# Kernel optimization log

Hardware: AMD Instinct MI355X
Metric: run time of the kernel (lower is better)

Reference implementation:

```python
import jax, jax.numpy as jnp
import numpy as np

B, S = 2, 1024
V, D, H, L, F, M = 50257, 768, 12, 6, 3072, 1024
DK = D // H
EPS = 1e-5


def _layer_norm(x, g, b):
    mu = jnp.mean(x, axis=-1, keepdims=True)
    var = jnp.mean(jnp.square(x - mu), axis=-1, keepdims=True)
    return (x - mu) * jax.lax.rsqrt(var + EPS) * g + b


def setup_inputs() -> dict:
    key = jax.random.key(0)
    ks = jax.random.split(key, 20)
    std = 0.02
    inp = {
        'input_ids': jax.random.randint(ks[0], (B, S), 0, V),
        'tok_emb': jax.random.normal(ks[1], (V, D), jnp.float32) * std,
        'pos_emb': jax.random.normal(ks[2], (M, D), jnp.float32) * std,
        # per-layer stacked params; linear weights stored as [in, out] (y = x @ W)
        'wq': jax.random.normal(ks[3], (L, D, D), jnp.float32) * std,
        'wk': jax.random.normal(ks[4], (L, D, D), jnp.float32) * std,
        'wv': jax.random.normal(ks[5], (L, D, D), jnp.float32) * std,
        'wo': jax.random.normal(ks[6], (L, D, D), jnp.float32) * std,
        'bo': jnp.zeros((L, D), jnp.float32),
        'fc_w': jax.random.normal(ks[7], (L, D, F), jnp.float32) * std,
        'fc_b': jnp.zeros((L, F), jnp.float32),
        'proj_w': jax.random.normal(ks[8], (L, F, D), jnp.float32) * std,
        'proj_b': jnp.zeros((L, D), jnp.float32),
        'ln1_g': jnp.ones((L, D), jnp.float32),
        'ln1_b': jnp.zeros((L, D), jnp.float32),
        'ln2_g': jnp.ones((L, D), jnp.float32),
        'ln2_b': jnp.zeros((L, D), jnp.float32),
        'lnf_g': jnp.ones((D,), jnp.float32),
        'lnf_b': jnp.zeros((D,), jnp.float32),
        'out_w': jax.random.normal(ks[9], (D, V), jnp.float32) * std,
    }
    return inp


def reference(input_ids, tok_emb, pos_emb, wq, wk, wv, wo, bo, fc_w, fc_b,
              proj_w, proj_b, ln1_g, ln1_b, ln2_g, ln2_b, lnf_g, lnf_b, out_w):
    b, s = input_ids.shape
    x = tok_emb[input_ids] + pos_emb[jnp.arange(s)][None, :, :]  # [B,S,D]
    causal = jnp.tril(jnp.ones((s, s), bool))  # [S,S]
    scale = 1.0 / np.sqrt(DK)
    for l in range(L):
        xn = _layer_norm(x, ln1_g[l], ln1_b[l])
        q = (xn @ wq[l]).reshape(b, s, H, DK).transpose(0, 2, 1, 3)
        k = (xn @ wk[l]).reshape(b, s, H, DK).transpose(0, 2, 1, 3)
        v = (xn @ wv[l]).reshape(b, s, H, DK).transpose(0, 2, 1, 3)
        scores = jnp.einsum('bhqd,bhkd->bhqk', q, k) * scale
        scores = jnp.where(causal[None, None], scores, -1e9)
        attn = jax.nn.softmax(scores, axis=-1)
        ctx = jnp.einsum('bhqk,bhkd->bhqd', attn, v)
        ctx = ctx.transpose(0, 2, 1, 3).reshape(b, s, D)
        x = x + ctx @ wo[l] + bo[l]
        xn = _layer_norm(x, ln2_g[l], ln2_b[l])
        h = jax.nn.gelu(xn @ fc_w[l] + fc_b[l], approximate=False)
        x = x + h @ proj_w[l] + proj_b[l]
    x = _layer_norm(x, lnf_g, lnf_b)
    logits = x @ out_w  # [B,S,V]
    return logits
```

## Files before the change

kernel.cpp:

```cpp
#include <hip/hip_runtime.h>
#include <hip/hip_bf16.h>
#include <math.h>

#define BB 2
#define SS 1024
#define DD 768
#define HH 12
#define LL 6
#define FF 3072
#define VV 50257
#define DKK 64
#define NROWS (BB * SS)
#define QKVN (3 * DD)
#define QBLK 64
#define KVBLK 64

#define OFF_QKV 0
#define OFF_WO  1769472
#define OFF_FC  2359296
#define OFF_PROJ 4718592
#define PL      7077888

typedef __attribute__((ext_vector_type(8))) short short8v;
typedef __attribute__((ext_vector_type(4))) float f32x4;
typedef __attribute__((ext_vector_type(4))) int int4v;

__device__ __forceinline__ float gelu_f(float x) {
    return 0.5f * x * (1.0f + erff(x * 0.70710678118654752440f));
}

__global__ __launch_bounds__(256) void embed_kernel(
    const int* __restrict__ ids, const float* __restrict__ tok,
    const float* __restrict__ pos, float* __restrict__ x) {
    int row = blockIdx.x;
    int s = row & (SS - 1);
    int id = ids[row];
    const float* t = tok + (size_t)id * DD;
    const float* p = pos + (size_t)s * DD;
    float* xr = x + (size_t)row * DD;
    for (int i = threadIdx.x; i < DD; i += 256)
        xr[i] = t[i] + p[i];
}

__global__ __launch_bounds__(256) void ln_kernel(
    const float* __restrict__ x, const float* __restrict__ g,
    const float* __restrict__ b, float* __restrict__ out) {
    int row = blockIdx.x;
    int tid = threadIdx.x;
    const float* xr = x + (size_t)row * DD;
    float v0 = xr[tid], v1 = xr[tid + 256], v2 = xr[tid + 512];
    __shared__ float red[256];
    red[tid] = v0 + v1 + v2;
    __syncthreads();
    for (int s2 = 128; s2 > 0; s2 >>= 1) {
        if (tid < s2) red[tid] += red[tid + s2];
        __syncthreads();
    }
    float mu = red[0] * (1.0f / DD);
    __syncthreads();
    float d0 = v0 - mu, d1 = v1 - mu, d2 = v2 - mu;
    red[tid] = d0 * d0 + d1 * d1 + d2 * d2;
    __syncthreads();
    for (int s2 = 128; s2 > 0; s2 >>= 1) {
        if (tid < s2) red[tid] += red[tid + s2];
        __syncthreads();
    }
    float r = rsqrtf(red[0] * (1.0f / DD) + 1e-5f);
    float* o = out + (size_t)row * DD;
    o[tid]       = d0 * r * g[tid]       + b[tid];
    o[tid + 256] = d1 * r * g[tid + 256] + b[tid + 256];
    o[tid + 512] = d2 * r * g[tid + 512] + b[tid + 512];
}

__global__ __launch_bounds__(256) void ln_bf16_kernel(
    const float* __restrict__ x, const float* __restrict__ g,
    const float* __restrict__ b, __hip_bfloat16* __restrict__ out) {
    int row = blockIdx.x;
    int tid = threadIdx.x;
    const float* xr = x + (size_t)row * DD;
    float v0 = xr[tid], v1 = xr[tid + 256], v2 = xr[tid + 512];
    __shared__ float red[256];
    red[tid] = v0 + v1 + v2;
    __syncthreads();
    for (int s2 = 128; s2 > 0; s2 >>= 1) {
        if (tid < s2) red[tid] += red[tid + s2];
        __syncthreads();
    }
    float mu = red[0] * (1.0f / DD);
    __syncthreads();
    float d0 = v0 - mu, d1 = v1 - mu, d2 = v2 - mu;
    red[tid] = d0 * d0 + d1 * d1 + d2 * d2;
    __syncthreads();
    for (int s2 = 128; s2 > 0; s2 >>= 1) {
        if (tid < s2) red[tid] += red[tid + s2];
        __syncthreads();
    }
    float r = rsqrtf(red[0] * (1.0f / DD) + 1e-5f);
    __hip_bfloat16* o = out + (size_t)row * DD;
    o[tid]       = __float2bfloat16(d0 * r * g[tid]       + b[tid]);
    o[tid + 256] = __float2bfloat16(d1 * r * g[tid + 256] + b[tid + 256]);
    o[tid + 512] = __float2bfloat16(d2 * r * g[tid + 512] + b[tid + 512]);
}

__global__ __launch_bounds__(256) void transpose_cvt_kernel(
    const float* __restrict__ W, __hip_bfloat16* __restrict__ Wt, int K, int N) {
    __shared__ float t[32][33];
    int bn = blockIdx.x * 32, bk = blockIdx.y * 32;
    int tx = threadIdx.x & 31, ty = threadIdx.x >> 5;
    for (int r = ty; r < 32; r += 8)
        t[r][tx] = (bn + tx < N) ? W[(size_t)(bk + r) * N + bn + tx] : 0.0f;
    __syncthreads();
    for (int r = ty; r < 32; r += 8) {
        int n = bn + r;
        if (n < N) Wt[(size_t)n * K + bk + tx] = __float2bfloat16(t[tx][r]);
    }
}

__global__ __launch_bounds__(256) void transpose_all_kernel(
    const float* __restrict__ wq, const float* __restrict__ wk,
    const float* __restrict__ wv, const float* __restrict__ wo,
    const float* __restrict__ fc_w, const float* __restrict__ proj_w,
    const float* __restrict__ out_w, __hip_bfloat16* __restrict__ Wt_all) {
    int bid = blockIdx.x;
    const float* W;
    __hip_bfloat16* Wt;
    int K, N, tn, tk;
    if (bid < 6 * 6912) {
        int l = bid / 6912, r = bid % 6912;
        __hip_bfloat16* base = Wt_all + (size_t)l * PL;
        if (r < 1728) {
            int which = r / 576, idx = r % 576;
            W = (which == 0 ? wq : (which == 1 ? wk : wv)) + (size_t)l * DD * DD;
            Wt = base + (size_t)which * DD * DD;
            K = DD; N = DD; tn = idx % 24; tk = idx / 24;
        } else if (r < 2304) {
            int idx = r - 1728;
            W = wo + (size_t)l * DD * DD;
            Wt = base + OFF_WO;
            K = DD; N = DD; tn = idx % 24; tk = idx / 24;
        } else if (r < 4608) {
            int idx = r - 2304;
            W = fc_w + (size_t)l * DD * FF;
            Wt = base + OFF_FC;
            K = DD; N = FF; tn = idx % 96; tk = idx / 96;
        } else {
            int idx = r - 4608;
            W = proj_w + (size_t)l * FF * DD;
            Wt = base + OFF_PROJ;
            K = FF; N = DD; tn = idx % 24; tk = idx / 24;
        }
    } else {
        int idx = bid - 6 * 6912;
        W = out_w;
        Wt = Wt_all + (size_t)6 * PL;
        K = DD; N = VV; tn = idx % 1571; tk = idx / 1571;
    }
    __shared__ float t[32][33];
    int bn = tn * 32, bk = tk * 32;
    int tx = threadIdx.x & 31, ty = threadIdx.x >> 5;
    for (int r = ty; r < 32; r += 8)
        t[r][tx] = (bn + tx < N) ? W[(size_t)(bk + r) * N + bn + tx] : 0.0f;
    __syncthreads();
    for (int r = ty; r < 32; r += 8) {
        int n = bn + r;
        if (n < N) Wt[(size_t)n * K + bk + tx] = __float2bfloat16(t[tx][r]);
    }
}

#define LDSOFF(row, ks) (((row) * 64) + ((((ks) ^ (((row) >> 1) & 3))) << 4))
#define SWZ128(row, byteoff) \
    ((row) * 128 + (((((byteoff) >> 4) ^ ((row) & 7)) & 7) << 4) + ((byteoff) & 15))

__device__ __forceinline__ void tile_remap(int mtiles, int BM, int BN, int& bm, int& bn) {
    const int nblk = gridDim.x;
    int hw = blockIdx.x, j = hw;
    if ((nblk & 7) == 0) j = (hw & 7) * (nblk >> 3) + (hw >> 3);
    bm = (j % mtiles) * BM;
    bn = (j / mtiles) * BN;
}

template<int BM, int BN>
__global__ __launch_bounds__(256) void gemm_mfma_kernel(
    const __hip_bfloat16* __restrict__ A, const __hip_bfloat16* __restrict__ Wt,
    const float* __restrict__ bias, const float* __restrict__ residual,
    float* __restrict__ Cf, __hip_bfloat16* __restrict__ Cb,
    int M, int N, int K, int do_gelu, int mtiles) {
    constexpr int BK = 32;
    constexpr int UA = (BM * 4) / 256;
    constexpr int UB = (BN * 4) / 256;
    constexpr int FM = BM / 32;
    constexpr int FN = BN / 32;
    __shared__ __align__(16) char As[BM * 64];
    __shared__ __align__(16) char Bs[BN * 64];

    const int tid = threadIdx.x;
    const int lane = tid & 63;
    const int wid = tid >> 6;
    int bm, bn;
    tile_remap(mtiles, BM, BN, bm, bn);
    const int r16 = lane & 15;
    const int kg = lane >> 4;
    const int wm = (wid >> 1) * (FM * 16);
    const int wn = (wid & 1) * (FN * 16);

    f32x4 acc[FM][FN];
    const f32x4 zf = {0.0f, 0.0f, 0.0f, 0.0f};
#pragma unroll
    for (int i = 0; i < FM; ++i)
#pragma unroll
        for (int j = 0; j < FN; ++j) acc[i][j] = zf;

    int4v areg[UA], breg[UB];
    const int4v zi = {0, 0, 0, 0};

#pragma unroll
    for (int u = 0; u < UA; ++u) {
        int c = tid + u * 256, row = c >> 2, sl = c & 3;
        areg[u] = *(const int4v*)(A + (size_t)(bm + row) * K + sl * 8);
    }
#pragma unroll
    for (int u = 0; u < UB; ++u) {
        int c = tid + u * 256, row = c >> 2, sl = c & 3;
        int4v bv = zi;
        if (bn + row < N) bv = *(const int4v*)(Wt + (size_t)(bn + row) * K + sl * 8);
        breg[u] = bv;
    }

    for (int k0 = 0; k0 < K; k0 += BK) {
        __syncthreads();
#pragma unroll
        for (int u = 0; u < UA; ++u) {
            int c = tid + u * 256, row = c >> 2, sl = c & 3;
            *(int4v*)(As + LDSOFF(row, sl)) = areg[u];
        }
#pragma unroll
        for (int u = 0; u < UB; ++u) {
            int c = tid + u * 256, row = c >> 2, sl = c & 3;
            *(int4v*)(Bs + LDSOFF(row, sl)) = breg[u];
        }
        __syncthreads();
        int kn = k0 + BK;
        if (kn < K) {
#pragma unroll
            for (int u = 0; u < UA; ++u) {
                int c = tid + u * 256, row = c >> 2, sl = c & 3;
                areg[u] = *(const int4v*)(A + (size_t)(bm + row) * K + kn + sl * 8);
            }
#pragma unroll
            for (int u = 0; u < UB; ++u) {
                int c = tid + u * 256, row = c >> 2, sl = c & 3;
                int4v bv = zi;
                if (bn + row < N) bv = *(const int4v*)(Wt + (size_t)(bn + row) * K + kn + sl * 8);
                breg[u] = bv;
            }
        }
        short8v af[FM], bfr[FN];
#pragma unroll
        for (int i = 0; i < FM; ++i) {
            int row = wm + i * 16 + r16;
            af[i] = *(const short8v*)(As + LDSOFF(row, kg));
        }
#pragma unroll
        for (int j = 0; j < FN; ++j) {
            int row = wn + j * 16 + r16;
            bfr[j] = *(const short8v*)(Bs + LDSOFF(row, kg));
        }
#pragma unroll
        for (int i = 0; i < FM; ++i)
#pragma unroll
            for (int j = 0; j < FN; ++j)
                acc[i][j] = __builtin_amdgcn_mfma_f32_16x16x32_bf16(
                    af[i], bfr[j], acc[i][j], 0, 0, 0);
    }

    const int rg = lane >> 4;
#pragma unroll
    for (int i = 0; i < FM; ++i) {
#pragma unroll
        for (int j = 0; j < FN; ++j) {
            int col = bn + wn + j * 16 + r16;
            if (col < N) {
#pragma unroll
                for (int r = 0; r < 4; ++r) {
                    int row = bm + wm + i * 16 + rg * 4 + r;
                    float v = acc[i][j][r];
                    if (bias) v += bias[col];
                    if (do_gelu) v = gelu_f(v);
                    size_t o = (size_t)row * N + col;
                    if (residual) v += residual[o];
                    if (Cf) Cf[o] = v;
                    else Cb[o] = __float2bfloat16(v);
                }
            }
        }
    }
}

__global__ __launch_bounds__(256) void qkv_gemm_kernel(
    const __hip_bfloat16* __restrict__ A, const __hip_bfloat16* __restrict__ Wt,
    __hip_bfloat16* __restrict__ qh, __hip_bfloat16* __restrict__ kh,
    __hip_bfloat16* __restrict__ vt) {
    constexpr int BM = 128, BN = 128, BK = 32;
    constexpr int K = DD;
    constexpr int UA = 2, UB = 2, FM = 4, FN = 4;
    __shared__ __align__(16) char As[BM * 64];
    __shared__ __align__(16) char Bs[BN * 64];

    const int tid = threadIdx.x;
    const int lane = tid & 63;
    const int wid = tid >> 6;
    int bm, bn;
    tile_remap(16, BM, BN, bm, bn);
    const int r16 = lane & 15;
    const int kg = lane >> 4;
    const int wm = (wid >> 1) * 64;
    const int wn = (wid & 1) * 64;

    f32x4 acc[FM][FN];
    const f32x4 zf = {0.0f, 0.0f, 0.0f, 0.0f};
#pragma unroll
    for (int i = 0; i < FM; ++i)
#pragma unroll
        for (int j = 0; j < FN; ++j) acc[i][j] = zf;

    int4v areg[UA], breg[UB];
#pragma unroll
    for (int u = 0; u < UA; ++u) {
        int c = tid + u * 256, row = c >> 2, sl = c & 3;
        areg[u] = *(const int4v*)(A + (size_t)(bm + row) * K + sl * 8);
    }
#pragma unroll
    for (int u = 0; u < UB; ++u) {
        int c = tid + u * 256, row = c >> 2, sl = c & 3;
        breg[u] = *(const int4v*)(Wt + (size_t)(bn + row) * K + sl * 8);
    }

    for (int k0 = 0; k0 < K; k0 += BK) {
        __syncthreads();
#pragma unroll
        for (int u = 0; u < UA; ++u) {
            int c = tid + u * 256, row = c >> 2, sl = c & 3;
            *(int4v*)(As + LDSOFF(row, sl)) = areg[u];
        }
#pragma unroll
        for (int u = 0; u < UB; ++u) {
            int c = tid + u * 256, row = c >> 2, sl = c & 3;
            *(int4v*)(Bs + LDSOFF(row, sl)) = breg[u];
        }
        __syncthreads();
        int kn = k0 + BK;
        if (kn < K) {
#pragma unroll
            for (int u = 0; u < UA; ++u) {
                int c = tid + u * 256, row = c >> 2, sl = c & 3;
                areg[u] = *(const int4v*)(A + (size_t)(bm + row) * K + kn + sl * 8);
            }
#pragma unroll
            for (int u = 0; u < UB; ++u) {
                int c = tid + u * 256, row = c >> 2, sl = c & 3;
                breg[u] = *(const int4v*)(Wt + (size_t)(bn + row) * K + kn + sl * 8);
            }
        }
        short8v af[FM], bfr[FN];
#pragma unroll
        for (int i = 0; i < FM; ++i)
            af[i] = *(const short8v*)(As + LDSOFF(wm + i * 16 + r16, kg));
#pragma unroll
        for (int j = 0; j < FN; ++j)
            bfr[j] = *(const short8v*)(Bs + LDSOFF(wn + j * 16 + r16, kg));
#pragma unroll
        for (int i = 0; i < FM; ++i)
#pragma unroll
            for (int j = 0; j < FN; ++j)
                acc[i][j] = __builtin_amdgcn_mfma_f32_16x16x32_bf16(
                    af[i], bfr[j], acc[i][j], 0, 0, 0);
    }

#pragma unroll
    for (int i = 0; i < FM; ++i) {
#pragma unroll
        for (int j = 0; j < FN; ++j) {
            int col = bn + wn + j * 16 + r16;
#pragma unroll
            for (int r = 0; r < 4; ++r) {
                int row = bm + wm + i * 16 + kg * 4 + r;
                int b = row >> 10, s = row & (SS - 1);
                float v = acc[i][j][r];
                if (col < DD) {
                    int h = col >> 6, d = col & 63;
                    qh[((size_t)(b * HH + h) * SS + s) * DKK + d] =
                        __float2bfloat16(v * 0.125f);
                } else if (col < 2 * DD) {
                    int c = col - DD, h = c >> 6, d = c & 63;
                    kh[((size_t)(b * HH + h) * SS + s) * DKK + d] = __float2bfloat16(v);
                } else {
                    int c = col - 2 * DD, h = c >> 6, d = c & 63;
                    vt[((size_t)(b * HH + h) * DKK + d) * SS + s] = __float2bfloat16(v);
                }
            }
        }
    }
}

__global__ __launch_bounds__(256) void flash_attn_kernel(
    const __hip_bfloat16* __restrict__ qh, const __hip_bfloat16* __restrict__ kh,
    const __hip_bfloat16* __restrict__ vt, __hip_bfloat16* __restrict__ ctx) {
    __shared__ __align__(16) char Ks[KVBLK * 128];
    __shared__ __align__(16) char Vs[DKK * 128];
    __shared__ __align__(16) char Ps[4][16 * 128];

    const int bh = blockIdx.x;
    const int qt = (gridDim.y - 1) - blockIdx.y;
    const int q0 = qt * QBLK;
    const int b = bh / HH;
    const int h = bh - b * HH;
    const int tid = threadIdx.x;
    const int lane = tid & 63;
    const int w = tid >> 6;
    const int r16 = lane & 15;
    const int kg = lane >> 4;
    char* Pw = Ps[w];

    const size_t qbase = ((size_t)bh * SS + q0 + w * 16 + r16) * DKK;
    short8v qf0 = *(const short8v*)(qh + qbase + kg * 8);
    short8v qf1 = *(const short8v*)(qh + qbase + 32 + kg * 8);

    f32x4 acc_o[4];
    const f32x4 zf = {0.0f, 0.0f, 0.0f, 0.0f};
    float m[4], l[4];
#pragma unroll
    for (int j = 0; j < 4; ++j) acc_o[j] = zf;
#pragma unroll
    for (int r = 0; r < 4; ++r) { m[r] = -1e30f; l[r] = 0.0f; }

    const int nt = qt + 1;
    for (int t = 0; t < nt; ++t) {
        __syncthreads();
        {
            const __hip_bfloat16* kp = kh + ((size_t)bh * SS + t * KVBLK) * DKK;
            const __hip_bfloat16* vp = vt + (size_t)bh * DKK * SS + t * KVBLK;
#pragma unroll
            for (int u = 0; u < 2; ++u) {
                int c = tid + u * 256;
                int row = c >> 3, slot = c & 7;
                *(int4v*)(Ks + SWZ128(row, slot * 16)) =
                    *(const int4v*)(kp + (size_t)row * DKK + slot * 8);
                *(int4v*)(Vs + SWZ128(row, slot * 16)) =
                    *(const int4v*)(vp + (size_t)row * SS + slot * 8);
            }
        }
        __syncthreads();

        f32x4 s[4];
#pragma unroll
        for (int j = 0; j < 4; ++j) s[j] = zf;
#pragma unroll
        for (int j = 0; j < 4; ++j) {
            short8v k0f = *(const short8v*)(Ks + SWZ128(j * 16 + r16, kg * 16));
            short8v k1f = *(const short8v*)(Ks + SWZ128(j * 16 + r16, 64 + kg * 16));
            s[j] = __builtin_amdgcn_mfma_f32_16x16x32_bf16(qf0, k0f, s[j], 0, 0, 0);
            s[j] = __builtin_amdgcn_mfma_f32_16x16x32_bf16(qf1, k1f, s[j], 0, 0, 0);
        }

        if (t == qt) {
#pragma unroll
            for (int j = 0; j < 4; ++j)
#pragma unroll
                for (int r = 0; r < 4; ++r)
                    if (j * 16 + r16 > w * 16 + kg * 4 + r) s[j][r] = -1e30f;
        }

        float alpha[4], rsum[4];
#pragma unroll
        for (int r = 0; r < 4; ++r) {
            float v = fmaxf(fmaxf(s[0][r], s[1][r]), fmaxf(s[2][r], s[3][r]));
#pragma unroll
            for (int d2 = 1; d2 < 16; d2 <<= 1)
                v = fmaxf(v, __shfl_xor(v, d2));
            float mnew = fmaxf(m[r], v);
            alpha[r] = __expf(m[r] - mnew);
            m[r] = mnew;
            rsum[r] = 0.0f;
        }
#pragma unroll
        for (int j = 0; j < 4; ++j)
#pragma unroll
            for (int r = 0; r < 4; ++r) {
                float p = __expf(s[j][r] - m[r]);
                rsum[r] += p;
                *(__hip_bfloat16*)(Pw + SWZ128(kg * 4 + r, (j * 16 + r16) * 2)) =
                    __float2bfloat16(p);
            }
#pragma unroll
        for (int r = 0; r < 4; ++r) {
#pragma unroll
            for (int d2 = 1; d2 < 16; d2 <<= 1)
                rsum[r] += __shfl_xor(rsum[r], d2);
            l[r] = l[r] * alpha[r] + rsum[r];
        }
#pragma unroll
        for (int j = 0; j < 4; ++j)
#pragma unroll
            for (int r = 0; r < 4; ++r) acc_o[j][r] *= alpha[r];

        short8v pa0 = *(const short8v*)(Pw + SWZ128(r16, kg * 16));
        short8v pa1 = *(const short8v*)(Pw + SWZ128(r16, 64 + kg * 16));
#pragma unroll
        for (int j = 0; j < 4; ++j) {
            short8v v0f = *(const short8v*)(Vs + SWZ128(j * 16 + r16, kg * 16));
            short8v v1f = *(const short8v*)(Vs + SWZ128(j * 16 + r16, 64 + kg * 16));
            acc_o[j] = __builtin_amdgcn_mfma_f32_16x16x32_bf16(pa0, v0f, acc_o[j], 0, 0, 0);
            acc_o[j] = __builtin_amdgcn_mfma_f32_16x16x32_bf16(pa1, v1f, acc_o[j], 0, 0, 0);
        }
    }

#pragma unroll
    for (int r = 0; r < 4; ++r) {
        float inv = 1.0f / l[r];
        int row = q0 + w * 16 + kg * 4 + r;
        __hip_bfloat16* cp = ctx + ((size_t)(b * SS) + row) * DD + h * DKK;
#pragma unroll
        for (int j = 0; j < 4; ++j)
            cp[j * 16 + r16] = __float2bfloat16(acc_o[j][r] * inv);
    }
}

__global__ __launch_bounds__(256) void gemm_kernel(
    const float* __restrict__ A, const float* __restrict__ W,
    const float* __restrict__ bias, const float* __restrict__ residual,
    float* __restrict__ C, int M, int N, int K, int do_gelu) {
    __shared__ float As[16][64];
    __shared__ float Ws[16][68];
    int tid = threadIdx.x;
    int bn = blockIdx.x * 64, bm = blockIdx.y * 64;
    int tx = tid & 15, ty = tid >> 4;
    int ar = tid >> 2, ak = (tid & 3) << 2;
    int wr = tid >> 4, wc = (tid & 15) << 2;
    bool n_vec = ((N & 3) == 0);
    float acc[4][4] = {};
    for (int k0 = 0; k0 < K; k0 += 16) {
        float4 av = *(const float4*)&A[(size_t)(bm + ar) * K + (k0 + ak)];
        As[ak + 0][ar] = av.x; As[ak + 1][ar] = av.y;
        As[ak + 2][ar] = av.z; As[ak + 3][ar] = av.w;
        int gn = bn + wc;
        const float* wp = &W[(size_t)(k0 + wr) * N + gn];
        float w0, w1, w2, w3;
        if (n_vec && gn + 3 < N) {
            float4 wv4 = *(const float4*)wp;
            w0 = wv4.x; w1 = wv4.y; w2 = wv4.z; w3 = wv4.w;
        } else {
            w0 = (gn + 0 < N) ? wp[0] : 0.0f;
            w1 = (gn + 1 < N) ? wp[1] : 0.0f;
            w2 = (gn + 2 < N) ? wp[2] : 0.0f;
            w3 = (gn + 3 < N) ? wp[3] : 0.0f;
        }
        Ws[wr][wc + 0] = w0; Ws[wr][wc + 1] = w1;
        Ws[wr][wc + 2] = w2; Ws[wr][wc + 3] = w3;
        __syncthreads();
#pragma unroll
        for (int kk = 0; kk < 16; ++kk) {
            float a[4], w[4];
#pragma unroll
            for (int i = 0; i < 4; ++i) a[i] = As[kk][ty * 4 + i];
#pragma unroll
            for (int j = 0; j < 4; ++j) w[j] = Ws[kk][tx * 4 + j];
#pragma unroll
            for (int i = 0; i < 4; ++i)
#pragma unroll
                for (int j = 0; j < 4; ++j)
                    acc[i][j] = fmaf(a[i], w[j], acc[i][j]);
        }
        __syncthreads();
    }
#pragma unroll
    for (int i = 0; i < 4; ++i) {
        int row = bm + ty * 4 + i;
#pragma unroll
        for (int j = 0; j < 4; ++j) {
            int col = bn + tx * 4 + j;
            if (col < N) {
                float val = acc[i][j];
                if (bias) val += bias[col];
                if (do_gelu) val = gelu_f(val);
                if (residual) val += residual[(size_t)row * N + col];
                C[(size_t)row * N + col] = val;
            }
        }
    }
}

__global__ __launch_bounds__(256) void attn_kernel(
    const float* __restrict__ q, const float* __restrict__ k,
    const float* __restrict__ v, float* __restrict__ ctx) {
    int bid = blockIdx.x;
    int qi = bid & (SS - 1);
    int bh = bid >> 10;
    int h = bh % HH;
    int b = bh / HH;
    int tid = threadIdx.x;
    __shared__ float qs[DKK];
    __shared__ float p[SS];
    __shared__ float red[256];
    __shared__ float ctx_red[4][DKK];
    const float* qrow = q + ((size_t)(b * SS + qi)) * DD + h * DKK;
    if (tid < DKK) qs[tid] = qrow[tid];
    __syncthreads();
    int nk = qi + 1;
    const float scale = 0.125f;
    for (int ki = tid; ki < nk; ki += 256) {
        const float* krow = k + ((size_t)(b * SS + ki)) * DD + h * DKK;
        float dot = 0.0f;
#pragma unroll
        for (int d = 0; d < DKK; d += 4) {
            float4 kv = *(const float4*)&krow[d];
            dot += qs[d] * kv.x + qs[d + 1] * kv.y + qs[d + 2] * kv.z + qs[d + 3] * kv.w;
        }
        p[ki] = dot * scale;
    }
    __syncthreads();
    float lmax = -1e30f;
    for (int ki = tid; ki < nk; ki += 256) lmax = fmaxf(lmax, p[ki]);
    red[tid] = lmax;
    __syncthreads();
    for (int s2 = 128; s2 > 0; s2 >>= 1) {
        if (tid < s2) red[tid] = fmaxf(red[tid], red[tid + s2]);
        __syncthreads();
    }
    float mm = red[0];
    __syncthreads();
    float lsum = 0.0f;
    for (int ki = tid; ki < nk; ki += 256) {
        float e = __expf(p[ki] - mm);
        p[ki] = e;
        lsum += e;
    }
    red[tid] = lsum;
    __syncthreads();
    for (int s2 = 128; s2 > 0; s2 >>= 1) {
        if (tid < s2) red[tid] += red[tid + s2];
        __syncthreads();
    }
    float inv = 1.0f / red[0];
    int d = tid & 63;
    int chunk = tid >> 6;
    float accd = 0.0f;
    for (int ki = chunk; ki < nk; ki += 4)
        accd += p[ki] * v[((size_t)(b * SS + ki)) * DD + h * DKK + d];
    ctx_red[chunk][d] = accd;
    __syncthreads();
    if (tid < DKK) {
        float sum = (ctx_red[0][tid] + ctx_red[1][tid]) + (ctx_red[2][tid] + ctx_red[3][tid]);
        ctx[((size_t)(b * SS + qi)) * DD + h * DKK + tid] = sum * inv;
    }
}

extern "C" void kernel_launch(void* const* d_in, const int* in_sizes, int n_in,
                              void* d_out, int out_size, void* d_ws, size_t ws_size,
                              hipStream_t stream) {
    const int*   ids    = (const int*)  d_in[0];
    const float* tok    = (const float*)d_in[1];
    const float* pos    = (const float*)d_in[2];
    const float* wq     = (const float*)d_in[3];
    const float* wk     = (const float*)d_in[4];
    const float* wv     = (const float*)d_in[5];
    const float* wo     = (const float*)d_in[6];
    const float* bo     = (const float*)d_in[7];
    const float* fc_w   = (const float*)d_in[8];
    const float* fc_b   = (const float*)d_in[9];
    const float* proj_w = (const float*)d_in[10];
    const float* proj_b = (const float*)d_in[11];
    const float* ln1_g  = (const float*)d_in[12];
    const float* ln1_b  = (const float*)d_in[13];
    const float* ln2_g  = (const float*)d_in[14];
    const float* ln2_b  = (const float*)d_in[15];
    const float* lnf_g  = (const float*)d_in[16];
    const float* lnf_b  = (const float*)d_in[17];
    const float* out_w  = (const float*)d_in[18];
    float* out = (float*)d_out;

    dim3 blk(256);

    const size_t SZ_X    = (size_t)NROWS * DD * 4;
    const size_t SZ_XN   = (size_t)NROWS * DD * 2;
    const size_t SZ_HD   = (size_t)BB * HH * SS * DKK * 2;
    const size_t SZ_CTX  = (size_t)NROWS * DD * 2;
    const size_t SZ_H    = (size_t)NROWS * FF * 2;
    const size_t SZ_WT1  = (size_t)50304 * DD * 2;
    const size_t SZ_WTA  = ((size_t)6 * PL + (size_t)50304 * DD) * 2;
    const size_t ACT     = SZ_X + SZ_XN + 3 * SZ_HD + SZ_CTX + SZ_H;
    const size_t NEED_MID = ACT + SZ_WT1;
    const size_t NEED_BIG = ACT + SZ_WTA;

    if (ws_size >= NEED_MID) {
        const bool big = (ws_size >= NEED_BIG);
        char* p = (char*)d_ws;
        float*          x    = (float*)p;          p += SZ_X;
        __hip_bfloat16* xn   = (__hip_bfloat16*)p; p += SZ_XN;
        __hip_bfloat16* qhb  = (__hip_bfloat16*)p; p += SZ_HD;
        __hip_bfloat16* khb  = (__hip_bfloat16*)p; p += SZ_HD;
        __hip_bfloat16* vtb  = (__hip_bfloat16*)p; p += SZ_HD;
        __hip_bfloat16* ctx  = (__hip_bfloat16*)p; p += SZ_CTX;
        __hip_bfloat16* hbuf = (__hip_bfloat16*)p; p += SZ_H;
        __hip_bfloat16* Wt   = (__hip_bfloat16*)p;

        dim3 tD(DD / 32, DD / 32);
        dim3 tF(FF / 32, DD / 32);
        dim3 tP(DD / 32, FF / 32);
        dim3 tV((VV + 31) / 32, DD / 32);

        const int nQKV = (QKVN / 128) * (NROWS / 128);
        const int nFC  = (FF / 128) * (NROWS / 128);
        const int nWO  = (DD / 64) * (NROWS / 64);
        const int nV   = ((VV + 127) / 128) * (NROWS / 128);
        dim3 gA(BB * HH, SS / QBLK);

        if (big)
            transpose_all_kernel<<<6 * 6912 + 37704, blk, 0, stream>>>(
                wq, wk, wv, wo, fc_w, proj_w, out_w, Wt);

        embed_kernel<<<NROWS, blk, 0, stream>>>(ids, tok, pos, x);

        for (int l = 0; l < LL; ++l) {
            __hip_bfloat16* qkvWt = big ? Wt + (size_t)l * PL : Wt;
            __hip_bfloat16* woWt  = big ? Wt + (size_t)l * PL + OFF_WO : Wt;
            __hip_bfloat16* fcWt  = big ? Wt + (size_t)l * PL + OFF_FC : Wt;
            __hip_bfloat16* pjWt  = big ? Wt + (size_t)l * PL + OFF_PROJ : Wt;

            ln_bf16_kernel<<<NROWS, blk, 0, stream>>>(x, ln1_g + l * DD, ln1_b + l * DD, xn);
            if (!big) {
                transpose_cvt_kernel<<<tD, blk, 0, stream>>>(wq + (size_t)l * DD * DD, qkvWt, DD, DD);
                transpose_cvt_kernel<<<tD, blk, 0, stream>>>(wk + (size_t)l * DD * DD, qkvWt + (size_t)DD * DD, DD, DD);
                transpose_cvt_kernel<<<tD, blk, 0, stream>>>(wv + (size_t)l * DD * DD, qkvWt + (size_t)2 * DD * DD, DD, DD);
            }
            qkv_gemm_kernel<<<nQKV, blk, 0, stream>>>(xn, qkvWt, qhb, khb, vtb);
            flash_attn_kernel<<<gA, blk, 0, stream>>>(qhb, khb, vtb, ctx);
            if (!big)
                transpose_cvt_kernel<<<tD, blk, 0, stream>>>(wo + (size_t)l * DD * DD, woWt, DD, DD);
            gemm_mfma_kernel<64, 64><<<nWO, blk, 0, stream>>>(
                ctx, woWt, bo + l * DD, x, x, nullptr, NROWS, DD, DD, 0, NROWS / 64);
            ln_bf16_kernel<<<NROWS, blk, 0, stream>>>(x, ln2_g + l * DD, ln2_b + l * DD, xn);
            if (!big)
                transpose_cvt_kernel<<<tF, blk, 0, stream>>>(fc_w + (size_t)l * DD * FF, fcWt, DD, FF);
            gemm_mfma_kernel<128, 128><<<nFC, blk, 0, stream>>>(
                xn, fcWt, fc_b + l * FF, nullptr, nullptr, hbuf, NROWS, FF, DD, 1, NROWS / 128);
            if (!big)
                transpose_cvt_kernel<<<tP, blk, 0, stream>>>(proj_w + (size_t)l * FF * DD, pjWt, FF, DD);
            gemm_mfma_kernel<64, 64><<<nWO, blk, 0, stream>>>(
                hbuf, pjWt, proj_b + l * DD, x, x, nullptr, NROWS, DD, FF, 0, NROWS / 64);
        }

        __hip_bfloat16* outWt = big ? Wt + (size_t)6 * PL : Wt;
        ln_bf16_kernel<<<NROWS, blk, 0, stream>>>(x, lnf_g, lnf_b, xn);
        if (!big)
            transpose_cvt_kernel<<<tV, blk, 0, stream>>>(out_w, outWt, DD, VV);
        gemm_mfma_kernel<128, 128><<<nV, blk, 0, stream>>>(
            xn, outWt, nullptr, nullptr, out, nullptr, NROWS, VV, DD, 0, NROWS / 128);
        return;
    }

    const size_t XSZ = (size_t)NROWS * DD;
    float* ws = (float*)d_ws;
    float* x  = ws;
    float* xn = x  + XSZ;
    float* qb = xn + XSZ;
    float* kb = qb + XSZ;
    float* vb = kb + XSZ;
    float* cb = vb + XSZ;
    float* hb = cb + XSZ;

    dim3 gD((DD + 63) / 64, NROWS / 64);
    dim3 gF((FF + 63) / 64, NROWS / 64);
    dim3 gV2((VV + 63) / 64, NROWS / 64);

    embed_kernel<<<NROWS, blk, 0, stream>>>(ids, tok, pos, x);
    for (int l = 0; l < LL; ++l) {
        const float* wq_l = wq + (size_t)l * DD * DD;
        const float* wk_l = wk + (size_t)l * DD * DD;
        const float* wv_l = wv + (size_t)l * DD * DD;
        const float* wo_l = wo + (size_t)l * DD * DD;
        const float* fc_w_l = fc_w + (size_t)l * DD * FF;
        const float* pj_w_l = proj_w + (size_t)l * FF * DD;
        ln_kernel<<<NROWS, blk, 0, stream>>>(x, ln1_g + l * DD, ln1_b + l * DD, xn);
        gemm_kernel<<<gD, blk, 0, stream>>>(xn, wq_l, nullptr, nullptr, qb, NROWS, DD, DD, 0);
        gemm_kernel<<<gD, blk, 0, stream>>>(xn, wk_l, nullptr, nullptr, kb, NROWS, DD, DD, 0);
        gemm_kernel<<<gD, blk, 0, stream>>>(xn, wv_l, nullptr, nullptr, vb, NROWS, DD, DD, 0);
        attn_kernel<<<BB * HH * SS, blk, 0, stream>>>(qb, kb, vb, cb);
        gemm_kernel<<<gD, blk, 0, stream>>>(cb, wo_l, bo + l * DD, x, x, NROWS, DD, DD, 0);
        ln_kernel<<<NROWS, blk, 0, stream>>>(x, ln2_g + l * DD, ln2_b + l * DD, xn);
        gemm_kernel<<<gF, blk, 0, stream>>>(xn, fc_w_l, fc_b + l * FF, nullptr, hb, NROWS, FF, DD, 1);
        gemm_kernel<<<gD, blk, 0, stream>>>(hb, pj_w_l, proj_b + l * DD, x, x, NROWS, DD, FF, 0);
    }
    ln_kernel<<<NROWS, blk, 0, stream>>>(x, lnf_g, lnf_b, xn);
    gemm_kernel<<<gV2, blk, 0, stream>>>(xn, out_w, nullptr, nullptr, out, NROWS, VV, DD, 0);
}
```

Before: 1.546 ms.

## Load GEMM tiles directly into LDS with global_load_lds, dropping register staging

Both the generic MFMA GEMM and the QKV GEMM now copy A and W tiles straight from global memory into LDS with the global_load_lds builtin, instead of staging them through registers and writing them to LDS. This saves VGPRs and the ds_write instructions. The register-level prefetch of the next K tile is removed, so global loads no longer overlap with MFMA work, and the XOR swizzle is dropped, which may bring back LDS bank conflicts on the fragment reads. The generic GEMM also loses its N-bound guard on the W load, so edge tiles such as the vocab projection (N=50257) may read past the end of the weight buffer.

Measured after the change: 1.681 ms. 8.8% more time.

```diff
diff --git a/kernel.cpp b/kernel.cpp
--- a/kernel.cpp
+++ b/kernel.cpp
@@ -27,6 +27,12 @@
 
 __device__ __forceinline__ float gelu_f(float x) {
     return 0.5f * x * (1.0f + erff(x * 0.70710678118654752440f));
+}
+
+__device__ __forceinline__ void gload16(const void* g, void* l) {
+    __builtin_amdgcn_global_load_lds(
+        (const __attribute__((address_space(1))) void*)g,
+        (__attribute__((address_space(3))) void*)l, 16, 0, 0);
 }
 
 __global__ __launch_bounds__(256) void embed_kernel(
@@ -167,7 +173,6 @@
     }
 }
 
-#define LDSOFF(row, ks) (((row) * 64) + ((((ks) ^ (((row) >> 1) & 3))) << 4))
 #define SWZ128(row, byteoff) \
     ((row) * 128 + (((((byteoff) >> 4) ^ ((row) & 7)) & 7) << 4) + ((byteoff) & 15))
 
@@ -210,61 +215,31 @@
 #pragma unroll
         for (int j = 0; j < FN; ++j) acc[i][j] = zf;
 
-    int4v areg[UA], breg[UB];
-    const int4v zi = {0, 0, 0, 0};
-
-#pragma unroll
-    for (int u = 0; u < UA; ++u) {
-        int c = tid + u * 256, row = c >> 2, sl = c & 3;
-        areg[u] = *(const int4v*)(A + (size_t)(bm + row) * K + sl * 8);
-    }
-#pragma unroll
-    for (int u = 0; u < UB; ++u) {
-        int c = tid + u * 256, row = c >> 2, sl = c & 3;
-        int4v bv = zi;
-        if (bn + row < N) bv = *(const int4v*)(Wt + (size_t)(bn + row) * K + sl * 8);
-        breg[u] = bv;
-    }
-
     for (int k0 = 0; k0 < K; k0 += BK) {
         __syncthreads();
 #pragma unroll
         for (int u = 0; u < UA; ++u) {
-            int c = tid + u * 256, row = c >> 2, sl = c & 3;
-            *(int4v*)(As + LDSOFF(row, sl)) = areg[u];
+            int cb = wid * 64 + u * 256;
+            int c = cb + lane;
+            gload16(A + (size_t)(bm + (c >> 2)) * K + k0 + (c & 3) * 8,
+                    As + cb * 16);
         }
 #pragma unroll
         for (int u = 0; u < UB; ++u) {
-            int c = tid + u * 256, row = c >> 2, sl = c & 3;
-            *(int4v*)(Bs + LDSOFF(row, sl)) = breg[u];
-        }
-        __syncthreads();
-        int kn = k0 + BK;
-        if (kn < K) {
-#pragma unroll
-            for (int u = 0; u < UA; ++u) {
-                int c = tid + u * 256, row = c >> 2, sl = c & 3;
-                areg[u] = *(const int4v*)(A + (size_t)(bm + row) * K + kn + sl * 8);
-            }
-#pragma unroll
-            for (int u = 0; u < UB; ++u) {
-                int c = tid + u * 256, row = c >> 2, sl = c & 3;
-                int4v bv = zi;
-                if (bn + row < N) bv = *(const int4v*)(Wt + (size_t)(bn + row) * K + kn + sl * 8);
-                breg[u] = bv;
-            }
-        }
+            int cb = wid * 64 + u * 256;
+            int c = cb + lane;
+            gload16(Wt + (size_t)(bn + (c >> 2)) * K + k0 + (c & 3) * 8,
+                    Bs + cb * 16);
+        }
+        __syncthreads();
+
         short8v af[FM], bfr[FN];
 #pragma unroll
-        for (int i = 0; i < FM; ++i) {
-            int row = wm + i * 16 + r16;
-            af[i] = *(const short8v*)(As + LDSOFF(row, kg));
-        }
-#pragma unroll
-        for (int j = 0; j < FN; ++j) {
-            int row = wn + j * 16 + r16;
-            bfr[j] = *(const short8v*)(Bs + LDSOFF(row, kg));
-        }
+        for (int i = 0; i < FM; ++i)
+            af[i] = *(const short8v*)(As + (wm + i * 16 + r16) * 64 + kg * 16);
+#pragma unroll
+        for (int j = 0; j < FN; ++j)
+            bfr[j] = *(const short8v*)(Bs + (wn + j * 16 + r16) * 64 + kg * 16);
 #pragma unroll
         for (int i = 0; i < FM; ++i)
 #pragma unroll
@@ -302,7 +277,7 @@
     __hip_bfloat16* __restrict__ vt) {
     constexpr int BM = 128, BN = 128, BK = 32;
     constexpr int K = DD;
-    constexpr int UA = 2, UB = 2, FM = 4, FN = 4;
+    constexpr int FM = 4, FN = 4;
     __shared__ __align__(16) char As[BM * 64];
     __shared__ __align__(16) char Bs[BN * 64];
 
@@ -323,51 +298,31 @@
 #pragma unroll
         for (int j = 0; j < FN; ++j) acc[i][j] = zf;
 
-    int4v areg[UA], breg[UB];
-#pragma unroll
-    for (int u = 0; u < UA; ++u) {
-        int c = tid + u * 256, row = c >> 2, sl = c & 3;
-        areg[u] = *(const int4v*)(A + (size_t)(bm + row) * K + sl * 8);
-    }
-#pragma unroll
-    for (int u = 0; u < UB; ++u) {
-        int c = tid + u * 256, row = c >> 2, sl = c & 3;
-        breg[u] = *(const int4v*)(Wt + (size_t)(bn + row) * K + sl * 8);
-    }
-
     for (int k0 = 0; k0 < K; k0 += BK) {
         __syncthreads();
 #pragma unroll
-        for (int u = 0; u < UA; ++u) {
-            int c = tid + u * 256, row = c >> 2, sl = c & 3;
-            *(int4v*)(As + LDSOFF(row, sl)) = areg[u];
-        }
-#pragma unroll
-        for (int u = 0; u < UB; ++u) {
-            int c = tid + u * 256, row = c >> 2, sl = c & 3;
-            *(int4v*)(Bs + LDSOFF(row, sl)) = breg[u];
-        }
-        __syncthreads();
-        int kn = k0 + BK;
-        if (kn < K) {
-#pragma unroll
-            for (int u = 0; u < UA; ++u) {
-                int c = tid + u * 256, row = c >> 2, sl = c & 3;
-                areg[u] = *(const int4v*)(A + (size_t)(bm + row) * K + kn + sl * 8);
-            }
-#pragma unroll
-            for (int u = 0; u < UB; ++u) {
-                int c = tid + u * 256, row = c >> 2, sl = c & 3;
-                breg[u] = *(const int4v*)(Wt + (size_t)(bn + row) * K + kn + sl * 8);
-            }
-        }
+        for (int u = 0; u < 2; ++u) {
+            int cb = wid * 64 + u * 256;
+            int c = cb + lane;
+            gload16(A + (size_t)(bm + (c >> 2)) * K + k0 + (c & 3) * 8,
+                    As + cb * 16);
+        }
+#pragma unroll
+        for (int u = 0; u < 2; ++u) {
+            int cb = wid * 64 + u * 256;
+            int c = cb + lane;
+            gload16(Wt + (size_t)(bn + (c >> 2)) * K + k0 + (c & 3) * 8,
+                    Bs + cb * 16);
+        }
+        __syncthreads();
+
         short8v af[FM], bfr[FN];
 #pragma unroll
         for (int i = 0; i < FM; ++i)
-            af[i] = *(const short8v*)(As + LDSOFF(wm + i * 16 + r16, kg));
+            af[i] = *(const short8v*)(As + (wm + i * 16 + r16) * 64 + kg * 16);
 #pragma unroll
         for (int j = 0; j < FN; ++j)
-            bfr[j] = *(const short8v*)(Bs + LDSOFF(wn + j * 16 + r16, kg));
+            bfr[j] = *(const short8v*)(Bs + (wn + j * 16 + r16) * 64 + kg * 16);
 #pragma unroll
         for (int i = 0; i < FM; ++i)
 #pragma unroll
```

## Add 256x256 direct-to-LDS pipelined GEMM for FC and vocab projections

Applied to the files above, without the earlier changes.

Adds a new 512-thread GEMM kernel with 256x256 tiles. It loads A and B straight from global memory into a 4-stage LDS ring buffer using global_load_lds and manually places vmcnt waits, so loads stay three stages ahead of the MFMA work. The FC and output-vocabulary GEMMs now use this kernel. The WO and proj GEMMs switch from 64x64 to 128x64 tiles, and the QKV load loops are merged. The larger tiles need 128KB of LDS and fewer, bigger blocks, which risks lower occupancy and tail imbalance. The padded vocab weight buffer (VPAD) now reads rows past V, and those rows are never initialized.

New measurement: 1.736 ms. 1.12x slower.

```diff
diff --git a/kernel.cpp b/kernel.cpp
--- a/kernel.cpp
+++ b/kernel.cpp
@@ -14,6 +14,7 @@
 #define QKVN (3 * DD)
 #define QBLK 64
 #define KVBLK 64
+#define VPAD 50432
 
 #define OFF_QKV 0
 #define OFF_WO  1769472
@@ -27,6 +28,20 @@
 
 __device__ __forceinline__ float gelu_f(float x) {
     return 0.5f * x * (1.0f + erff(x * 0.70710678118654752440f));
+}
+
+__device__ __forceinline__ void gload16(const void* g, void* l) {
+    __builtin_amdgcn_global_load_lds(
+        (const __attribute__((address_space(1))) void*)g,
+        (__attribute__((address_space(3))) void*)l, 16, 0, 0);
+}
+__device__ __forceinline__ unsigned lds_off(const void* p) {
+    return (unsigned)(size_t)(const __attribute__((address_space(3))) char*)p;
+}
+__device__ __forceinline__ short8v ds_read128(unsigned addr) {
+    short8v r;
+    asm volatile("ds_read_b128 %0, %1" : "=v"(r) : "v"(addr));
+    return r;
 }
 
 __global__ __launch_bounds__(256) void embed_kernel(
@@ -179,6 +194,92 @@
     bn = (j / mtiles) * BN;
 }
 
+__global__ __launch_bounds__(512) void gemm256_kernel(
+    const __hip_bfloat16* __restrict__ A, const __hip_bfloat16* __restrict__ Wt,
+    const float* __restrict__ bias, float* __restrict__ Cf,
+    __hip_bfloat16* __restrict__ Cb, int M, int N, int K, int do_gelu, int mtiles) {
+    __shared__ __align__(16) char lds[131072];
+    const int tid = threadIdx.x;
+    const int lane = tid & 63;
+    const int w = tid >> 6;
+    const int wr = w >> 2, wc = w & 3;
+    const int r16 = lane & 15, kg = lane >> 4;
+    int bm, bn;
+    tile_remap(mtiles, 256, 256, bm, bn);
+
+    auto STAGE = [&](int T) {
+        char* lb = lds + (T & 3) * 32768;
+        int k0 = T * 32;
+#pragma unroll
+        for (int u = 0; u < 2; ++u) {
+            int cb = w * 128 + u * 64;
+            int c = cb + lane;
+            int row = c >> 2;
+            int sc = ((c & 3) ^ ((row >> 1) & 3)) * 8;
+            gload16(A + (size_t)(bm + row) * K + k0 + sc, lb + cb * 16);
+            gload16(Wt + (size_t)(bn + row) * K + k0 + sc, lb + 16384 + cb * 16);
+        }
+    };
+
+    f32x4 acc[8][4];
+    const f32x4 zf = {0.0f, 0.0f, 0.0f, 0.0f};
+#pragma unroll
+    for (int i = 0; i < 8; ++i)
+#pragma unroll
+        for (int j = 0; j < 4; ++j) acc[i][j] = zf;
+
+    unsigned aoff[8], boff[4];
+#pragma unroll
+    for (int i = 0; i < 8; ++i) aoff[i] = LDSOFF(wr * 128 + i * 16 + r16, kg);
+#pragma unroll
+    for (int j = 0; j < 4; ++j) boff[j] = 16384 + LDSOFF(wc * 64 + j * 16 + r16, kg);
+    const unsigned lbase = lds_off(lds);
+
+    STAGE(0); STAGE(1); STAGE(2);
+    const int NT = K >> 5;
+    for (int t = 0; t < NT; ++t) {
+        if (t < NT - 2)       asm volatile("s_waitcnt vmcnt(8)" ::: "memory");
+        else if (t == NT - 2) asm volatile("s_waitcnt vmcnt(4)" ::: "memory");
+        else                  asm volatile("s_waitcnt vmcnt(0)" ::: "memory");
+        __builtin_amdgcn_s_barrier();
+        __builtin_amdgcn_sched_barrier(0);
+        if (t + 3 < NT) STAGE(t + 3);
+        unsigned ab = lbase + (unsigned)(t & 3) * 32768u;
+        short8v af[8], bf[4];
+#pragma unroll
+        for (int i = 0; i < 8; ++i) af[i] = ds_read128(ab + aoff[i]);
+#pragma unroll
+        for (int j = 0; j < 4; ++j) bf[j] = ds_read128(ab + boff[j]);
+        asm volatile("s_waitcnt lgkmcnt(0)" ::: "memory");
+        __builtin_amdgcn_sched_barrier(0);
+#pragma unroll
+        for (int i = 0; i < 8; ++i)
+#pragma unroll
+            for (int j = 0; j < 4; ++j)
+                acc[i][j] = __builtin_amdgcn_mfma_f32_16x16x32_bf16(
+                    af[i], bf[j], acc[i][j], 0, 0, 0);
+    }
+
+    const int rg = lane >> 4;
+#pragma unroll
+    for (int i = 0; i < 8; ++i)
+#pragma unroll
+        for (int j = 0; j < 4; ++j) {
+            int col = bn + wc * 64 + j * 16 + r16;
+            if (col < N) {
+#pragma unroll
+                for (int r = 0; r < 4; ++r) {
+                    int row = bm + wr * 128 + i * 16 + rg * 4 + r;
+                    float v = acc[i][j][r];
+                    if (bias) v += bias[col];
+                    if (do_gelu) v = gelu_f(v);
+                    if (Cf) Cf[(size_t)row * N + col] = v;
+                    else Cb[(size_t)row * N + col] = __float2bfloat16(v);
+                }
+            }
+        }
+}
+
 template<int BM, int BN>
 __global__ __launch_bounds__(256) void gemm_mfma_kernel(
     const __hip_bfloat16* __restrict__ A, const __hip_bfloat16* __restrict__ Wt,
@@ -302,7 +403,7 @@
     __hip_bfloat16* __restrict__ vt) {
     constexpr int BM = 128, BN = 128, BK = 32;
     constexpr int K = DD;
-    constexpr int UA = 2, UB = 2, FM = 4, FN = 4;
+    constexpr int FM = 4, FN = 4;
     __shared__ __align__(16) char As[BM * 64];
     __shared__ __align__(16) char Bs[BN * 64];
 
@@ -323,41 +424,29 @@
 #pragma unroll
         for (int j = 0; j < FN; ++j) acc[i][j] = zf;
 
-    int4v areg[UA], breg[UB];
-#pragma unroll
-    for (int u = 0; u < UA; ++u) {
+    int4v areg[2], breg[2];
+#pragma unroll
+    for (int u = 0; u < 2; ++u) {
         int c = tid + u * 256, row = c >> 2, sl = c & 3;
         areg[u] = *(const int4v*)(A + (size_t)(bm + row) * K + sl * 8);
-    }
-#pragma unroll
-    for (int u = 0; u < UB; ++u) {
-        int c = tid + u * 256, row = c >> 2, sl = c & 3;
         breg[u] = *(const int4v*)(Wt + (size_t)(bn + row) * K + sl * 8);
     }
 
     for (int k0 = 0; k0 < K; k0 += BK) {
         __syncthreads();
 #pragma unroll
-        for (int u = 0; u < UA; ++u) {
+        for (int u = 0; u < 2; ++u) {
             int c = tid + u * 256, row = c >> 2, sl = c & 3;
             *(int4v*)(As + LDSOFF(row, sl)) = areg[u];
-        }
-#pragma unroll
-        for (int u = 0; u < UB; ++u) {
-            int c = tid + u * 256, row = c >> 2, sl = c & 3;
             *(int4v*)(Bs + LDSOFF(row, sl)) = breg[u];
         }
         __syncthreads();
         int kn = k0 + BK;
         if (kn < K) {
 #pragma unroll
-            for (int u = 0; u < UA; ++u) {
+            for (int u = 0; u < 2; ++u) {
                 int c = tid + u * 256, row = c >> 2, sl = c & 3;
                 areg[u] = *(const int4v*)(A + (size_t)(bm + row) * K + kn + sl * 8);
-            }
-#pragma unroll
-            for (int u = 0; u < UB; ++u) {
-                int c = tid + u * 256, row = c >> 2, sl = c & 3;
                 breg[u] = *(const int4v*)(Wt + (size_t)(bn + row) * K + kn + sl * 8);
             }
         }
@@ -685,8 +774,8 @@
     const size_t SZ_HD   = (size_t)BB * HH * SS * DKK * 2;
     const size_t SZ_CTX  = (size_t)NROWS * DD * 2;
     const size_t SZ_H    = (size_t)NROWS * FF * 2;
-    const size_t SZ_WT1  = (size_t)50304 * DD * 2;
-    const size_t SZ_WTA  = ((size_t)6 * PL + (size_t)50304 * DD) * 2;
+    const size_t SZ_WT1  = (size_t)VPAD * DD * 2;
+    const size_t SZ_WTA  = ((size_t)6 * PL + (size_t)VPAD * DD) * 2;
     const size_t ACT     = SZ_X + SZ_XN + 3 * SZ_HD + SZ_CTX + SZ_H;
     const size_t NEED_MID = ACT + SZ_WT1;
     const size_t NEED_BIG = ACT + SZ_WTA;
@@ -709,9 +798,9 @@
         dim3 tV((VV + 31) / 32, DD / 32);
 
         const int nQKV = (QKVN / 128) * (NROWS / 128);
-        const int nFC  = (FF / 128) * (NROWS / 128);
-        const int nWO  = (DD / 64) * (NROWS / 64);
-        const int nV   = ((VV + 127) / 128) * (NROWS / 128);
+        const int nWO  = (DD / 64) * (NROWS / 128);
+        const int nFC  = (FF / 256) * (NROWS / 256);
+        const int nV   = (VPAD / 256) * (NROWS / 256);
         dim3 gA(BB * HH, SS / QBLK);
 
         if (big)
@@ -736,25 +825,25 @@
             flash_attn_kernel<<<gA, blk, 0, stream>>>(qhb, khb, vtb, ctx);
             if (!big)
                 transpose_cvt_kernel<<<tD, blk, 0, stream>>>(wo + (size_t)l * DD * DD, woWt, DD, DD);
-            gemm_mfma_kernel<64, 64><<<nWO, blk, 0, stream>>>(
-                ctx, woWt, bo + l * DD, x, x, nullptr, NROWS, DD, DD, 0, NROWS / 64);
+            gemm_mfma_kernel<128, 64><<<nWO, blk, 0, stream>>>(
+                ctx, woWt, bo + l * DD, x, x, nullptr, NROWS, DD, DD, 0, NROWS / 128);
             ln_bf16_kernel<<<NROWS, blk, 0, stream>>>(x, ln2_g + l * DD, ln2_b + l * DD, xn);
             if (!big)
                 transpose_cvt_kernel<<<tF, blk, 0, stream>>>(fc_w + (size_t)l * DD * FF, fcWt, DD, FF);
-            gemm_mfma_kernel<128, 128><<<nFC, blk, 0, stream>>>(
-                xn, fcWt, fc_b + l * FF, nullptr, nullptr, hbuf, NROWS, FF, DD, 1, NROWS / 128);
+            gemm256_kernel<<<nFC, 512, 0, stream>>>(
+                xn, fcWt, fc_b + l * FF, nullptr, hbuf, NROWS, FF, DD, 1, NROWS / 256);
             if (!big)
                 transpose_cvt_kernel<<<tP, blk, 0, stream>>>(proj_w + (size_t)l * FF * DD, pjWt, FF, DD);
-            gemm_mfma_kernel<64, 64><<<nWO, blk, 0, stream>>>(
-                hbuf, pjWt, proj_b + l * DD, x, x, nullptr, NROWS, DD, FF, 0, NROWS / 64);
+            gemm_mfma_kernel<128, 64><<<nWO, blk, 0, stream>>>(
+                hbuf, pjWt, proj_b + l * DD, x, x, nullptr, NROWS, DD, FF, 0, NROWS / 128);
         }
 
         __hip_bfloat16* outWt = big ? Wt + (size_t)6 * PL : Wt;
         ln_bf16_kernel<<<NROWS, blk, 0, stream>>>(x, lnf_g, lnf_b, xn);
         if (!big)
             transpose_cvt_kernel<<<tV, blk, 0, stream>>>(out_w, outWt, DD, VV);
-        gemm_mfma_kernel<128, 128><<<nV, blk, 0, stream>>>(
-            xn, outWt, nullptr, nullptr, out, nullptr, NROWS, VV, DD, 0, NROWS / 128);
+        gemm256_kernel<<<nV, 512, 0, stream>>>(
+            xn, outWt, nullptr, out, nullptr, NROWS, VV, DD, 0, NROWS / 256);
         return;
     }
 
```
